# Kernel tuning notes

Measured on AMD Instinct MI355X. Metric: run time of the kernel, lower is better.

Reference implementation:

```python
import jax, jax.numpy as jnp
import numpy as np
from jax import lax

DT = 0.01
INPUT_SCALER = 20.0
BETA1 = 1.0


def setup_inputs() -> dict:
    key = jax.random.key(0)
    k1, k2, k3 = jax.random.split(key, 3)
    bs, T, d, nk = 8, 64, 32, 32
    X_r = jax.random.normal(k1, (bs, T, d, d, nk), dtype=jnp.float32)
    X_i = jax.random.normal(k2, (bs, T, d, d, nk), dtype=jnp.float32)
    # omegas ~ U(min_omega, max_omega) * 2*pi (Gaussian blur omitted: it only
    # smooths the fixed parameter initialization, not the forward math)
    min_omega, max_omega = 0.1, 1.0
    omegas = (jax.random.uniform(k3, (d, d, nk), dtype=jnp.float32)
              * (max_omega - min_omega) + min_omega) * (2 * 3.1415)
    return {"X_r": X_r, "X_i": X_i, "omegas": omegas}


def reference(X_r, X_i, omegas):
    bs, T, d1, d2, nk = X_r.shape
    # time-major for scan: [T, bs, d, d, nk]
    Xr_t = jnp.moveaxis(X_r, 1, 0)
    Xi_t = jnp.moveaxis(X_i, 1, 0)

    r0 = jnp.ones((bs, d1, d2, nk), dtype=X_r.dtype)
    phi0 = jnp.zeros((bs, d1, d2, nk), dtype=X_r.dtype)

    def step(carry, xs):
        r, phi = carry
        xr, xi = xs
        input_r = INPUT_SCALER * xr * jnp.cos(phi)
        input_phi = INPUT_SCALER * xi * jnp.sin(phi)
        r = r + ((1.0 - BETA1 * r * r) * r + input_r) * DT
        phi = phi + (omegas - input_phi) * DT
        return (r, phi), (r, phi)

    _, (r_arr, phi_arr) = lax.scan(step, (r0, phi0), (Xr_t, Xi_t))
    # back to batch-major: [bs, T, d, d, nk]
    r_arr = jnp.moveaxis(r_arr, 0, 1)
    phi_arr = jnp.moveaxis(phi_arr, 0, 1)
    return r_arr * jnp.cos(phi_arr), r_arr * jnp.sin(phi_arr)
```

## Files before the change

### kernel.cpp

```cpp
#include <hip/hip_runtime.h>


#define T_STEPS 64
#define CHV2    16384
#define BS      8
#define DEPTH   16

typedef float v2f __attribute__((ext_vector_type(2)));

__global__ __launch_bounds__(256)
void hopf_scan_kernel(const float* __restrict__ Xr,
                      const float* __restrict__ Xi,
                      const float* __restrict__ Om,
                      float* __restrict__ out)
{
    const float DT = 0.01f;
    const float SC = 20.0f;
    const float S1 = -1.6666667e-1f, S2 = 8.3333333e-3f,
                S3 = -1.9841270e-4f, S4 = 2.7557319e-6f;
    const float C1 = -0.5f, C2 = 4.1666667e-2f,
                C3 = -1.3888889e-3f, C4 = 2.4801587e-5f;

    const v2f* __restrict__ vXr = (const v2f*)Xr;
    const v2f* __restrict__ vXi = (const v2f*)Xi;
    const v2f* __restrict__ vOm = (const v2f*)Om;
    v2f* __restrict__ vout      = (v2f*)out;

    int tid = blockIdx.x * blockDim.x + threadIdx.x;
    int b   = tid >> 14;
    int cv  = tid & (CHV2 - 1);

    v2f om = vOm[cv];

    const size_t stride = CHV2;
    size_t base = (size_t)(b * T_STEPS) * stride + cv;
    const v2f* pxr = vXr + base;
    const v2f* pxi = vXi + base;
    v2f* po0 = vout + base;
    v2f* po1 = po0 + (size_t)BS * T_STEPS * stride;

    float r[2]  = {1.f, 1.f};
    float co[2] = {1.f, 1.f};
    float si[2] = {0.f, 0.f};

    v2f xr[DEPTH], xi[DEPTH];
    #pragma unroll
    for (int i = 0; i < DEPTH; ++i) {
        xr[i] = pxr[(size_t)i * stride];
        xi[i] = pxi[(size_t)i * stride];
    }

    #pragma unroll
    for (int t = 0; t < T_STEPS; ++t) {
        const int s = t & (DEPTH - 1);
        v2f axr = xr[s];
        v2f axi = xi[s];
        if (t + DEPTH < T_STEPS) {
            xr[s] = pxr[(size_t)(t + DEPTH) * stride];
            xi[s] = pxi[(size_t)(t + DEPTH) * stride];
        }

        v2f o0, o1;
        #pragma unroll
        for (int j = 0; j < 2; ++j) {
            float ir   = SC * axr[j] * co[j];
            float dphi = (om[j] - SC * axi[j] * si[j]) * DT;
            r[j] = r[j] + ((1.f - r[j] * r[j]) * r[j] + ir) * DT;

            float u  = dphi * dphi;
            float sp = fmaf(u, S4, S3);
            sp = fmaf(u, sp, S2);
            sp = fmaf(u, sp, S1);
            sp = fmaf(u, sp, 1.f);
            sp *= dphi;
            float cp = fmaf(u, C4, C3);
            cp = fmaf(u, cp, C2);
            cp = fmaf(u, cp, C1);
            cp = fmaf(u, cp, 1.f);

            float nco = fmaf(co[j], cp, -si[j] * sp);
            float nsi = fmaf(si[j], cp,  co[j] * sp);
            co[j] = nco; si[j] = nsi;

            o0[j] = r[j] * co[j];
            o1[j] = r[j] * si[j];
        }

        size_t off = (size_t)t * stride;
        po0[off] = o0;
        po1[off] = o1;
    }
}

extern "C" void kernel_launch(void* const* d_in, const int* in_sizes, int n_in,
                              void* d_out, int out_size, void* d_ws, size_t ws_size,
                              hipStream_t stream) {
    const float* Xr = (const float*)d_in[0];
    const float* Xi = (const float*)d_in[1];
    const float* Om = (const float*)d_in[2];
    float* out = (float*)d_out;

    dim3 block(256);
    dim3 grid(BS * CHV2 / 256);
    hopf_scan_kernel<<<grid, block, 0, stream>>>(Xr, Xi, Om, out);
}
```

Before: 238.9 us.

## Hand-schedule prefetch pipeline with inline asm loads, explicit vmcnt waits, nt stores

Replaces the compiler-scheduled prefetch ring with inline-asm global loads and stores, unrolled by template recursion. Each step waits on an explicit s_waitcnt vmcnt count so that only the oldest load pair must have arrived, which keeps the other loads in flight. Output stores use the nontemporal hint, the prefetch depth goes from 16 to 12 and launch bounds request 2 blocks per CU. The hand-counted vmcnt values must match the real number of outstanding memory ops, including the stores. If they do not, data may be read before it arrives or the waits may stall too long.

```diff
diff --git a/kernel.cpp b/kernel.cpp
--- a/kernel.cpp
+++ b/kernel.cpp
@@ -4,68 +4,60 @@
 #define T_STEPS 64
 #define CHV2    16384
 #define BS      8
-#define DEPTH   16
+#define DEPTH   12
 
 typedef float v2f __attribute__((ext_vector_type(2)));
 
-__global__ __launch_bounds__(256)
-void hopf_scan_kernel(const float* __restrict__ Xr,
-                      const float* __restrict__ Xi,
-                      const float* __restrict__ Om,
-                      float* __restrict__ out)
+template<int i>
+__device__ __forceinline__ void prime_loads(const v2f* pxr, const v2f* pxi,
+                                            v2f (&xr)[DEPTH], v2f (&xi)[DEPTH])
 {
-    const float DT = 0.01f;
-    const float SC = 20.0f;
-    const float S1 = -1.6666667e-1f, S2 = 8.3333333e-3f,
-                S3 = -1.9841270e-4f, S4 = 2.7557319e-6f;
-    const float C1 = -0.5f, C2 = 4.1666667e-2f,
-                C3 = -1.3888889e-3f, C4 = 2.4801587e-5f;
+    if constexpr (i < DEPTH) {
+        asm volatile("global_load_dwordx2 %0, %1, off"
+                     : "=v"(xr[i]) : "v"(pxr + (size_t)i * CHV2));
+        asm volatile("global_load_dwordx2 %0, %1, off"
+                     : "=v"(xi[i]) : "v"(pxi + (size_t)i * CHV2));
+        prime_loads<i + 1>(pxr, pxi, xr, xi);
+    }
+}
 
-    const v2f* __restrict__ vXr = (const v2f*)Xr;
-    const v2f* __restrict__ vXi = (const v2f*)Xi;
-    const v2f* __restrict__ vOm = (const v2f*)Om;
-    v2f* __restrict__ vout      = (v2f*)out;
+template<int t>
+__device__ __forceinline__ void steps(const v2f* pxr, const v2f* pxi,
+                                      v2f* po0, v2f* po1,
+                                      const float (&om)[2],
+                                      float (&r)[2], float (&co)[2], float (&si)[2],
+                                      v2f (&xr)[DEPTH], v2f (&xi)[DEPTH])
+{
+    if constexpr (t < T_STEPS) {
+        const float DTS = 0.01f;
+        const float SC  = 20.0f;
+        const float S1 = -1.6666667e-1f, S2 = 8.3333333e-3f,
+                    S3 = -1.9841270e-4f, S4 = 2.7557319e-6f;
+        const float C1 = -0.5f, C2 = 4.1666667e-2f,
+                    C3 = -1.3888889e-3f, C4 = 2.4801587e-5f;
 
-    int tid = blockIdx.x * blockDim.x + threadIdx.x;
-    int b   = tid >> 14;
-    int cv  = tid & (CHV2 - 1);
+        constexpr int s = t % DEPTH;
+        constexpr int N = (t < DEPTH) ? (2 * DEPTH - 2 + 2 * t)
+                        : (t <= T_STEPS - DEPTH) ? (4 * DEPTH - 2)
+                        : (4 * DEPTH - 2 - 2 * (t - (T_STEPS - DEPTH)));
+        asm volatile("s_waitcnt vmcnt(%0)" :: "i"(N));
+        __builtin_amdgcn_sched_barrier(0);
 
-    v2f om = vOm[cv];
-
-    const size_t stride = CHV2;
-    size_t base = (size_t)(b * T_STEPS) * stride + cv;
-    const v2f* pxr = vXr + base;
-    const v2f* pxi = vXi + base;
-    v2f* po0 = vout + base;
-    v2f* po1 = po0 + (size_t)BS * T_STEPS * stride;
-
-    float r[2]  = {1.f, 1.f};
-    float co[2] = {1.f, 1.f};
-    float si[2] = {0.f, 0.f};
-
-    v2f xr[DEPTH], xi[DEPTH];
-    #pragma unroll
-    for (int i = 0; i < DEPTH; ++i) {
-        xr[i] = pxr[(size_t)i * stride];
-        xi[i] = pxi[(size_t)i * stride];
-    }
-
-    #pragma unroll
-    for (int t = 0; t < T_STEPS; ++t) {
-        const int s = t & (DEPTH - 1);
         v2f axr = xr[s];
         v2f axi = xi[s];
-        if (t + DEPTH < T_STEPS) {
-            xr[s] = pxr[(size_t)(t + DEPTH) * stride];
-            xi[s] = pxi[(size_t)(t + DEPTH) * stride];
+        if constexpr (t + DEPTH < T_STEPS) {
+            asm volatile("global_load_dwordx2 %0, %1, off"
+                         : "=v"(xr[s]) : "v"(pxr + (size_t)(t + DEPTH) * CHV2));
+            asm volatile("global_load_dwordx2 %0, %1, off"
+                         : "=v"(xi[s]) : "v"(pxi + (size_t)(t + DEPTH) * CHV2));
         }
 
         v2f o0, o1;
         #pragma unroll
         for (int j = 0; j < 2; ++j) {
             float ir   = SC * axr[j] * co[j];
-            float dphi = (om[j] - SC * axi[j] * si[j]) * DT;
-            r[j] = r[j] + ((1.f - r[j] * r[j]) * r[j] + ir) * DT;
+            float dphi = (om[j] - SC * axi[j] * si[j]) * DTS;
+            r[j] = r[j] + ((1.f - r[j] * r[j]) * r[j] + ir) * DTS;
 
             float u  = dphi * dphi;
             float sp = fmaf(u, S4, S3);
@@ -86,10 +78,49 @@
             o1[j] = r[j] * si[j];
         }
 
-        size_t off = (size_t)t * stride;
-        po0[off] = o0;
-        po1[off] = o1;
+        asm volatile("global_store_dwordx2 %0, %1, off nt"
+                     :: "v"(po0 + (size_t)t * CHV2), "v"(o0));
+        asm volatile("global_store_dwordx2 %0, %1, off nt"
+                     :: "v"(po1 + (size_t)t * CHV2), "v"(o1));
+
+        steps<t + 1>(pxr, pxi, po0, po1, om, r, co, si, xr, xi);
     }
+}
+
+__global__ __launch_bounds__(256, 2)
+void hopf_scan_kernel(const float* __restrict__ Xr,
+                      const float* __restrict__ Xi,
+                      const float* __restrict__ Om,
+                      float* __restrict__ out)
+{
+    const v2f* __restrict__ vXr = (const v2f*)Xr;
+    const v2f* __restrict__ vXi = (const v2f*)Xi;
+    const v2f* __restrict__ vOm = (const v2f*)Om;
+    v2f* __restrict__ vout      = (v2f*)out;
+
+    int tid = blockIdx.x * blockDim.x + threadIdx.x;
+    int b   = tid >> 14;
+    int cv  = tid & (CHV2 - 1);
+
+    v2f omv = vOm[cv];
+    float om[2] = {omv[0], omv[1]};
+    asm volatile("" :: "v"(om[0]), "v"(om[1]));
+
+    const size_t stride = CHV2;
+    size_t base = (size_t)(b * T_STEPS) * stride + cv;
+    const v2f* pxr = vXr + base;
+    const v2f* pxi = vXi + base;
+    v2f* po0 = vout + base;
+    v2f* po1 = po0 + (size_t)BS * T_STEPS * stride;
+
+    float r[2]  = {1.f, 1.f};
+    float co[2] = {1.f, 1.f};
+    float si[2] = {0.f, 0.f};
+
+    v2f xr[DEPTH], xi[DEPTH];
+    prime_loads<0>(pxr, pxi, xr, xi);
+
+    steps<0>(pxr, pxi, po0, po1, om, r, co, si, xr, xi);
 }
 
 extern "C" void kernel_launch(void* const* d_in, const int* in_sizes, int n_in,
```

Result: no change. 238.3 us (-0.3%).
